# Kernel optimization log

Measured on AMD Instinct MI355X. Metric: run time of the kernel, lower is better.

Reference implementation:

```python
import jax, jax.numpy as jnp
import numpy as np

THRESHOLD = 0.5
EPS = 1e-6


def setup_inputs() -> dict:
    key = jax.random.key(0)
    k1, k2, k3 = jax.random.split(key, 3)
    B, C, T = 32, 6, 64
    K, N = 8, 128
    S, P = 32, 64
    points = jax.random.normal(k1, (B, C, T, 2), dtype=jnp.float32)
    road_boundary = jax.random.normal(k2, (B, K, N, 2), dtype=jnp.float32)
    centerlines = jax.random.normal(k3, (B, S, P, 2), dtype=jnp.float32)
    return {"points": points, "road_boundary": road_boundary, "centerlines": centerlines}


def _cross(v1, v2):
    return v1[..., 0] * v2[..., 1] - v1[..., 1] * v2[..., 0]


def reference(points, road_boundary, centerlines):
    B, C, T, _ = points.shape
    _, K, N, _ = road_boundary.shape
    _, S, P, _ = centerlines.shape

    # --- min distance to boundary segments ---
    seg_a = road_boundary[:, :, :-1, :]          # (B,K,N-1,2)
    seg_d = road_boundary[:, :, 1:, :] - seg_a   # (B,K,N-1,2)

    p = points[:, None, :, :, None, :]           # (B,1,C,T,1,2)
    a = seg_a[:, :, None, None, :, :]            # (B,K,1,1,N-1,2)
    d = seg_d[:, :, None, None, :, :]            # (B,K,1,1,N-1,2)

    v1 = p - a                                   # (B,K,C,T,N-1,2)
    dot = (v1 * d).sum(-1)                       # (B,K,C,T,N-1)
    edge_sq = (d * d).sum(-1)                    # (B,K,1,1,N-1)
    proj = jnp.clip(dot / (edge_sq + EPS), 0.0, 1.0)
    closest = a + d * proj[..., None]            # (B,K,C,T,N-1,2)
    dist = jnp.sqrt(((p - closest) ** 2).sum(-1))  # (B,K,C,T,N-1)
    min_dist = dist.min(axis=-1).min(axis=1)     # (B,C,T)

    # --- nearest centerline point ---
    cl = centerlines.reshape(B, S * P, 2)        # (B,SP,2)
    v2 = points[:, None, :, :, :] - cl[:, :, None, None, :]  # (B,SP,C,T,2)
    cl_dist_sq = (v2 ** 2).sum(-1)               # (B,SP,C,T)
    idx = jnp.argmin(cl_dist_sq, axis=1)         # (B,C,T)
    closest_cl = cl[jnp.arange(B)[:, None, None], idx]  # (B,C,T,2)

    # --- segment intersection test: (point -> nearest centerline pt) vs boundary edges ---
    a1 = points[:, None, None, :, :, :]          # (B,1,1,C,T,2)
    a2 = closest_cl[:, None, None, :, :, :]      # (B,1,1,C,T,2)
    b1 = seg_a[:, :, :, None, None, :]           # (B,K,N-1,1,1,2)
    db = seg_d[:, :, :, None, None, :]           # (B,K,N-1,1,1,2)

    da = a2 - a1
    dp = a1 - b1                                 # (B,K,N-1,C,T,2)
    dadb = _cross(da, db)                        # (B,K,N-1,C,T)
    t = _cross(da, dp) / (dadb + EPS)
    u = _cross(db, dp) / (dadb + EPS)
    intersect = (t >= 0.0) & (t <= 1.0) & (u >= 0.0) & (u <= 1.0)

    inside = ~jnp.any(intersect, axis=(1, 2))    # (B,C,T)
    min_dist = jnp.where(inside, -min_dist, min_dist)
    return jax.nn.relu(min_dist + THRESHOLD).sum(-1)  # (B,C)
```

## Files before the change

### kernel.cpp

```cpp
#include <hip/hip_runtime.h>

constexpr int cB = 32, cC = 6, cT = 64;
constexpr int cK = 8, cN = 128;
constexpr int cS = 32, cP = 64;
constexpr int NSEG_PAD = cK * cN;
constexpr int NCL  = cS * cP;
constexpr int G = 8;
constexpr int LPP = 32;
constexpr float F_EPS = 1e-6f;
constexpr float F_THRESHOLD = 0.5f;

__global__ __launch_bounds__(256) void offroad_kernel(
    const float* __restrict__ points,
    const float* __restrict__ road_boundary,
    const float* __restrict__ centerlines,
    float* __restrict__ out)
{
    __shared__ float4 s_seg[NSEG_PAD];
    __shared__ float4 s_cl4[NCL / 2];

    const int blk = blockIdx.x;
    const int g  = blk & (G - 1);
    const int bc = blk >> 3;
    const int b  = bc / cC;
    const int tid = threadIdx.x;

    const float qnan = __int_as_float(0x7fc00000);

    const float2* rb2 = (const float2*)(road_boundary + (size_t)b * cK * cN * 2);
    for (int s = tid; s < NSEG_PAD; s += 256) {
        int n = s & (cN - 1);
        if (n < cN - 1) {
            float2 a  = rb2[s];
            float2 nx = rb2[s + 1];
            s_seg[s] = make_float4(a.x, a.y, nx.x - a.x, nx.y - a.y);
        } else {
            s_seg[s] = make_float4(qnan, qnan, qnan, qnan);
        }
    }
    const float4* cl4 = (const float4*)(centerlines + (size_t)b * NCL * 2);
    for (int i = tid; i < NCL / 2; i += 256) s_cl4[i] = cl4[i];
    __syncthreads();

    const int t = (g << 3) | (tid >> 5);
    const int q = tid & (LPP - 1);
    const size_t pbase = (((size_t)bc) * cT + t) * 2;
    const float px = points[pbase + 0];
    const float py = points[pbase + 1];

    float min_d2 = 3.4e38f;
    float best_d2 = 3.4e38f;
    int best_i = 0x7fffffff;
    #pragma unroll 4
    for (int i = 0; i < NSEG_PAD / LPP; ++i) {
        int s = q + i * LPP;
        float4 sg = s_seg[s];
        float v1x = px - sg.x, v1y = py - sg.y;
        float dot = v1x * sg.z + v1y * sg.w;
        float e2  = sg.z * sg.z + sg.w * sg.w + F_EPS;
        float proj = dot * __builtin_amdgcn_rcpf(e2);
        proj = fminf(fmaxf(proj, 0.0f), 1.0f);
        float ex = v1x - sg.z * proj;
        float ey = v1y - sg.w * proj;
        float d2 = ex * ex + ey * ey;
        min_d2 = fminf(min_d2, d2);

        int j = q + i * LPP;
        float4 cp = s_cl4[j];
        float dxa = px - cp.x, dya = py - cp.y;
        float d2a = dxa * dxa + dya * dya;
        float dxb = px - cp.z, dyb = py - cp.w;
        float d2b = dxb * dxb + dyb * dyb;
        int   ia = 2 * j;
        float dmin = d2a; int imin = ia;
        if (d2b < d2a) { dmin = d2b; imin = ia + 1; }
        if (dmin < best_d2 || (dmin == best_d2 && imin < best_i)) {
            best_d2 = dmin; best_i = imin;
        }
    }
    #pragma unroll
    for (int off = 1; off <= 16; off <<= 1) {
        float od2 = __shfl_xor(best_d2, off);
        int   oi  = __shfl_xor(best_i, off);
        if (od2 < best_d2 || (od2 == best_d2 && oi < best_i)) {
            best_d2 = od2; best_i = oi;
        }
    }
    const float2* s_cl2 = (const float2*)s_cl4;
    const float2 cc = s_cl2[best_i];

    const float dax = cc.x - px, day = cc.y - py;
    int hit = 0;
    #pragma unroll 4
    for (int i = 0; i < NSEG_PAD / LPP; ++i) {
        int s = q + i * LPP;
        float4 sg = s_seg[s];
        float dpx = px - sg.x, dpy = py - sg.y;
        float dadb = dax * sg.w - day * sg.z;
        float inv = __builtin_amdgcn_rcpf(dadb + F_EPS);
        float tt = (dax * dpy - day * dpx) * inv;
        float uu = (sg.z * dpy - sg.w * dpx) * inv;
        hit |= (tt >= 0.0f && tt <= 1.0f && uu >= 0.0f && uu <= 1.0f) ? 1 : 0;
    }

    #pragma unroll
    for (int off = 1; off <= 16; off <<= 1) {
        min_d2 = fminf(min_d2, __shfl_xor(min_d2, off));
        hit |= __shfl_xor(hit, off);
    }

    float md = sqrtf(min_d2);
    float sd = hit ? md : -md;
    float val = fmaxf(sd + F_THRESHOLD, 0.0f);
    if (q != 0) val = 0.0f;

    #pragma unroll
    for (int off = 32; off >= 1; off >>= 1)
        val += __shfl_down(val, off);
    if ((tid & 63) == 0)
        atomicAdd(&out[bc], val);
}

extern "C" void kernel_launch(void* const* d_in, const int* in_sizes, int n_in,
                              void* d_out, int out_size, void* d_ws, size_t ws_size,
                              hipStream_t stream) {
    const float* points      = (const float*)d_in[0];
    const float* boundary    = (const float*)d_in[1];
    const float* centerlines = (const float*)d_in[2];
    float* out = (float*)d_out;
    hipMemsetAsync(out, 0, (size_t)out_size * sizeof(float), stream);
    offroad_kernel<<<cB * cC * G, 256, 0, stream>>>(points, boundary, centerlines, out);
}
```

Measured before the change: 99.42 us.

## Read boundary and centerline data directly from global memory instead of LDS staging

Removes the shared-memory staging of segments and centerline points and the block-wide barrier. Each thread now loads segment endpoints and centerline pairs straight from global memory (through the cache) and recomputes segment deltas in the loop. Padding segments are handled by clamping the next index and masking the intersection hit. Launch bounds now ask for 8 blocks per CU. The aim is to cut the per-block staging prologue and barrier. The cost is repeated global/L1 loads and extra address and delta arithmetic in the inner loops.

```diff
diff --git a/kernel.cpp b/kernel.cpp
--- a/kernel.cpp
+++ b/kernel.cpp
@@ -10,37 +10,22 @@
 constexpr float F_EPS = 1e-6f;
 constexpr float F_THRESHOLD = 0.5f;
 
-__global__ __launch_bounds__(256) void offroad_kernel(
+__global__ __launch_bounds__(256, 8) void offroad_kernel(
     const float* __restrict__ points,
     const float* __restrict__ road_boundary,
     const float* __restrict__ centerlines,
     float* __restrict__ out)
 {
-    __shared__ float4 s_seg[NSEG_PAD];
-    __shared__ float4 s_cl4[NCL / 2];
-
     const int blk = blockIdx.x;
     const int g  = blk & (G - 1);
     const int bc = blk >> 3;
     const int b  = bc / cC;
     const int tid = threadIdx.x;
 
-    const float qnan = __int_as_float(0x7fc00000);
-
-    const float2* rb2 = (const float2*)(road_boundary + (size_t)b * cK * cN * 2);
-    for (int s = tid; s < NSEG_PAD; s += 256) {
-        int n = s & (cN - 1);
-        if (n < cN - 1) {
-            float2 a  = rb2[s];
-            float2 nx = rb2[s + 1];
-            s_seg[s] = make_float4(a.x, a.y, nx.x - a.x, nx.y - a.y);
-        } else {
-            s_seg[s] = make_float4(qnan, qnan, qnan, qnan);
-        }
-    }
-    const float4* cl4 = (const float4*)(centerlines + (size_t)b * NCL * 2);
-    for (int i = tid; i < NCL / 2; i += 256) s_cl4[i] = cl4[i];
-    __syncthreads();
+    const float2* __restrict__ rb2 =
+        (const float2*)(road_boundary + (size_t)b * cK * cN * 2);
+    const float4* __restrict__ cl4 =
+        (const float4*)(centerlines + (size_t)b * NCL * 2);
 
     const int t = (g << 3) | (tid >> 5);
     const int q = tid & (LPP - 1);
@@ -48,30 +33,32 @@
     const float px = points[pbase + 0];
     const float py = points[pbase + 1];
 
-    float min_d2 = 3.4e38f;
+    float min_d2  = 3.4e38f;
     float best_d2 = 3.4e38f;
-    int best_i = 0x7fffffff;
+    int   best_i  = 0x7fffffff;
     #pragma unroll 4
     for (int i = 0; i < NSEG_PAD / LPP; ++i) {
-        int s = q + i * LPP;
-        float4 sg = s_seg[s];
-        float v1x = px - sg.x, v1y = py - sg.y;
-        float dot = v1x * sg.z + v1y * sg.w;
-        float e2  = sg.z * sg.z + sg.w * sg.w + F_EPS;
+        const int s = q + i * LPP;
+        const int n = s & (cN - 1);
+        const int s1 = s + ((n < cN - 1) ? 1 : 0);
+        float2 a  = rb2[s];
+        float2 nx = rb2[s1];
+        float dx = nx.x - a.x, dy = nx.y - a.y;
+        float v1x = px - a.x,  v1y = py - a.y;
+        float dot = v1x * dx + v1y * dy;
+        float e2  = dx * dx + dy * dy + F_EPS;
         float proj = dot * __builtin_amdgcn_rcpf(e2);
         proj = fminf(fmaxf(proj, 0.0f), 1.0f);
-        float ex = v1x - sg.z * proj;
-        float ey = v1y - sg.w * proj;
-        float d2 = ex * ex + ey * ey;
-        min_d2 = fminf(min_d2, d2);
+        float ex = v1x - dx * proj;
+        float ey = v1y - dy * proj;
+        min_d2 = fminf(min_d2, ex * ex + ey * ey);
 
-        int j = q + i * LPP;
-        float4 cp = s_cl4[j];
+        float4 cp = cl4[s];
         float dxa = px - cp.x, dya = py - cp.y;
         float d2a = dxa * dxa + dya * dya;
         float dxb = px - cp.z, dyb = py - cp.w;
         float d2b = dxb * dxb + dyb * dyb;
-        int   ia = 2 * j;
+        int   ia = 2 * s;
         float dmin = d2a; int imin = ia;
         if (d2b < d2a) { dmin = d2b; imin = ia + 1; }
         if (dmin < best_d2 || (dmin == best_d2 && imin < best_i)) {
@@ -86,21 +73,25 @@
             best_d2 = od2; best_i = oi;
         }
     }
-    const float2* s_cl2 = (const float2*)s_cl4;
-    const float2 cc = s_cl2[best_i];
+    const float2 cc = ((const float2*)cl4)[best_i];
 
     const float dax = cc.x - px, day = cc.y - py;
     int hit = 0;
     #pragma unroll 4
     for (int i = 0; i < NSEG_PAD / LPP; ++i) {
-        int s = q + i * LPP;
-        float4 sg = s_seg[s];
-        float dpx = px - sg.x, dpy = py - sg.y;
-        float dadb = dax * sg.w - day * sg.z;
+        const int s = q + i * LPP;
+        const int n = s & (cN - 1);
+        const int s1 = s + ((n < cN - 1) ? 1 : 0);
+        float2 a  = rb2[s];
+        float2 nx = rb2[s1];
+        float dbx = nx.x - a.x, dby = nx.y - a.y;
+        float dpx = px - a.x,   dpy = py - a.y;
+        float dadb = dax * dby - day * dbx;
         float inv = __builtin_amdgcn_rcpf(dadb + F_EPS);
         float tt = (dax * dpy - day * dpx) * inv;
-        float uu = (sg.z * dpy - sg.w * dpx) * inv;
-        hit |= (tt >= 0.0f && tt <= 1.0f && uu >= 0.0f && uu <= 1.0f) ? 1 : 0;
+        float uu = (dbx * dpy - dby * dpx) * inv;
+        bool inb = (tt >= 0.0f) & (tt <= 1.0f) & (uu >= 0.0f) & (uu <= 1.0f);
+        hit |= (int)((n < cN - 1) & inb);
     }
 
     #pragma unroll
```

After: 98.69 us. About the same (-0.7%).
